# Kernel tuning notes

Measured on AMD Instinct MI355X. Metric: run time of the kernel, lower is better.

## Reference

```python
import jax, jax.numpy as jnp
import numpy as np

N_NODES = 50000
N_EDGES = 800000
IN_CH = 1024
OUT_CH = 256


def setup_inputs() -> dict:
    key = jax.random.key(0)
    ks = jax.random.split(key, 7)
    x = jax.random.normal(ks[0], (N_NODES, IN_CH), dtype=jnp.float32)
    src_index = jax.random.randint(ks[1], (N_EDGES,), 0, N_NODES, dtype=jnp.int32)
    tar_index = jax.random.randint(ks[2], (N_EDGES,), 0, N_NODES, dtype=jnp.int32)
    edge_weight = jax.random.uniform(ks[3], (N_EDGES,), dtype=jnp.float32)
    self_edge_weight = jax.random.uniform(ks[4], (N_NODES,), dtype=jnp.float32)
    # Linear layer params (torch.nn.Linear: y = x @ W.T + b)
    bound = 1.0 / np.sqrt(IN_CH)
    W = jax.random.uniform(ks[5], (OUT_CH, IN_CH), dtype=jnp.float32, minval=-bound, maxval=bound)
    b = jax.random.uniform(ks[6], (OUT_CH,), dtype=jnp.float32, minval=-bound, maxval=bound)
    return {"x": x, "W": W, "b": b, "src_index": src_index, "tar_index": tar_index,
            "edge_weight": edge_weight, "self_edge_weight": self_edge_weight}


def reference(x, W, b, src_index, tar_index, edge_weight, self_edge_weight):
    # dense linear projection: [N, in] -> [N, out]
    h = jnp.einsum('ni,oi->no', x, W) + b
    # edge aggregation: out[t] += w_e * h[src_e]  (SpMM-like gather/scatter)
    msgs = h[src_index] * edge_weight[:, None]          # [E, out]
    agg = jax.ops.segment_sum(msgs, tar_index, num_segments=h.shape[0])
    # self-loop term
    return agg + self_edge_weight[:, None] * h
```

## Files before the change

### kernel.cpp

```cpp
#include <hip/hip_runtime.h>
#include <hip/hip_bf16.h>

#define N_NODES 50000
#define N_EDGES 800000
#define IN_CH 1024
#define OUT_CH 256
#define NBLK 196

typedef __attribute__((ext_vector_type(8))) short bf16x8;
typedef __attribute__((ext_vector_type(4))) float f32x4;

__device__ inline unsigned short f2bf(float f) {
  union { float f; unsigned int u; } v; v.f = f;
  unsigned int r = v.u + 0x7fffu + ((v.u >> 16) & 1u);
  return (unsigned short)(r >> 16);
}
__device__ inline float bf2f(unsigned short u) {
  union { unsigned int u; float f; } v; v.u = ((unsigned int)u) << 16;
  return v.f;
}
__device__ inline unsigned int cvtpk_bf16(float a, float b) {
  unsigned int r;
  asm("v_cvt_pk_bf16_f32 %0, %1, %2" : "=v"(r) : "v"(a), "v"(b));
  return r;
}

#define GLOAD16(SRC, DST)                                                      \
  __builtin_amdgcn_global_load_lds(                                            \
      (const __attribute__((address_space(1))) void*)(SRC),                    \
      (__attribute__((address_space(3))) void*)(DST), 16, 0, 0)

__global__ __launch_bounds__(256) void prep_hist(const float* __restrict__ W,
                                                 unsigned short* __restrict__ Wb,
                                                 const int* __restrict__ tar,
                                                 int* __restrict__ counts) {
  const int b = blockIdx.x, t = threadIdx.x;
  if (b < 256) {
    const int i4 = (b * 256 + t) * 4;
    float4 f = *(const float4*)(W + i4);
    *(ushort4*)(Wb + i4) = make_ushort4(f2bf(f.x), f2bf(f.y), f2bf(f.z), f2bf(f.w));
  } else {
    const int e = (b - 256) * 256 + t;
    if (e < N_EDGES) atomicAdd(&counts[tar[e]], 1);
  }
}

__global__ __launch_bounds__(256, 3) void gemm_proj(
    const float* __restrict__ X, const unsigned short* __restrict__ Wb,
    const float* __restrict__ bias, unsigned short* __restrict__ Hb)
{
  __shared__ float lds_a[2][128][32];
  __shared__ unsigned short lds_b[2][128][32];

  const int tid  = threadIdx.x;
  const int lane = tid & 63;
  const int w    = tid >> 6;
  const int wr   = w >> 1, wc = w & 1;
  const int gm0  = blockIdx.x * 128;
  const int gn0  = blockIdx.y * 128;

  f32x4 acc[4][4];
  #pragma unroll
  for (int i = 0; i < 4; i++)
    #pragma unroll
    for (int j = 0; j < 4; j++) acc[i][j] = (f32x4)0.0f;

#define STAGE(BUF, K0)                                                         \
  {                                                                            \
    _Pragma("unroll")                                                          \
    for (int q = 0; q < 4; q++) {                                              \
      const int wl   = w * 4 + q;                                              \
      const int row  = 8 * wl + (lane >> 3);                                   \
      const int grow = gm0 + row;                                              \
      const int sc   = (lane & 7) ^ (row & 7);                                 \
      if (grow < N_NODES)                                                      \
        GLOAD16(X + (size_t)grow * IN_CH + (K0) + sc * 4,                      \
                &lds_a[BUF][8 * wl][0]);                                       \
    }                                                                          \
    _Pragma("unroll")                                                          \
    for (int q = 0; q < 2; q++) {                                              \
      const int wl  = w * 2 + q;                                               \
      const int row = 16 * wl + (lane >> 2);                                   \
      const int sc  = (lane & 3) ^ (row & 3);                                  \
      GLOAD16(Wb + (size_t)(gn0 + row) * IN_CH + (K0) + sc * 8,                \
              &lds_b[BUF][16 * wl][0]);                                        \
    }                                                                          \
  }

#define COMPUTE(BUF)                                                           \
  {                                                                            \
    const int l15 = lane & 15;                                                 \
    const int kb  = lane >> 4;                                                 \
    bf16x8 af[4], bfr[4];                                                      \
    _Pragma("unroll")                                                          \
    for (int i = 0; i < 4; i++) {                                              \
      const int row = wr * 64 + i * 16 + l15;                                  \
      const int c0  = (2 * kb) ^ (row & 7);                                    \
      const int c1  = (2 * kb + 1) ^ (row & 7);                                \
      f32x4 lo = *(const f32x4*)&lds_a[BUF][row][c0 * 4];                      \
      f32x4 hi = *(const f32x4*)&lds_a[BUF][row][c1 * 4];                      \
      union { unsigned int u[4]; bf16x8 v; } t;                                \
      t.u[0] = cvtpk_bf16(lo[0], lo[1]);                                       \
      t.u[1] = cvtpk_bf16(lo[2], lo[3]);                                       \
      t.u[2] = cvtpk_bf16(hi[0], hi[1]);                                       \
      t.u[3] = cvtpk_bf16(hi[2], hi[3]);                                       \
      af[i] = t.v;                                                             \
    }                                                                          \
    _Pragma("unroll")                                                          \
    for (int j = 0; j < 4; j++) {                                              \
      const int row = wc * 64 + j * 16 + l15;                                  \
      const int c   = kb ^ (row & 3);                                          \
      bfr[j] = *(const bf16x8*)&lds_b[BUF][row][c * 8];                        \
    }                                                                          \
    _Pragma("unroll")                                                          \
    for (int i = 0; i < 4; i++)                                                \
      _Pragma("unroll")                                                        \
      for (int j = 0; j < 4; j++)                                              \
        acc[i][j] = __builtin_amdgcn_mfma_f32_16x16x32_bf16(af[i], bfr[j],     \
                                                            acc[i][j], 0, 0, 0); \
  }

  STAGE(0, 0);
  __syncthreads();

  for (int ks = 0; ks < 32; ks += 2) {
    if (ks + 1 < 32) STAGE(1, (ks + 1) * 32);
    COMPUTE(0);
    __syncthreads();
    if (ks + 2 < 32) STAGE(0, (ks + 2) * 32);
    COMPUTE(1);
    __syncthreads();
  }
#undef STAGE
#undef COMPUTE

  float bj[4];
  #pragma unroll
  for (int j = 0; j < 4; j++)
    bj[j] = bias[gn0 + wc * 64 + j * 16 + (lane & 15)];

  #pragma unroll
  for (int i = 0; i < 4; i++) {
    const int grow_base = gm0 + wr * 64 + i * 16 + ((lane >> 4) << 2);
    #pragma unroll
    for (int r = 0; r < 4; r++) {
      const int grow = grow_base + r;
      if (grow < N_NODES) {
        #pragma unroll
        for (int j = 0; j < 4; j++) {
          const int gcol = gn0 + wc * 64 + j * 16 + (lane & 15);
          Hb[(size_t)grow * OUT_CH + gcol] = f2bf(acc[i][j][r] + bj[j]);
        }
      }
    }
  }
}

__global__ __launch_bounds__(256) void scan_block(const int* __restrict__ counts,
                                                  int* __restrict__ offsets,
                                                  int* __restrict__ blocksum) {
  __shared__ int wsum[4];
  const int tid = threadIdx.x, lane = tid & 63, wv = tid >> 6;
  const int i = blockIdx.x * 256 + tid;
  const int v = (i < N_NODES) ? counts[i] : 0;
  int s = v;
  #pragma unroll
  for (int off = 1; off < 64; off <<= 1) {
    int t = __shfl_up(s, off, 64);
    if (lane >= off) s += t;
  }
  if (lane == 63) wsum[wv] = s;
  __syncthreads();
  if (tid == 0) {
    int c = 0;
    #pragma unroll
    for (int k = 0; k < 4; k++) { int t = wsum[k]; wsum[k] = c; c += t; }
  }
  __syncthreads();
  const int excl = wsum[wv] + s - v;
  if (i < N_NODES) offsets[i] = excl;
  if (tid == 255) blocksum[blockIdx.x] = excl + v;
}

__global__ __launch_bounds__(256) void scan_sums(int* __restrict__ blocksum,
                                                 int* __restrict__ offsets) {
  __shared__ int wsum[4];
  const int tid = threadIdx.x, lane = tid & 63, wv = tid >> 6;
  const int v = (tid < NBLK) ? blocksum[tid] : 0;
  int s = v;
  #pragma unroll
  for (int off = 1; off < 64; off <<= 1) {
    int t = __shfl_up(s, off, 64);
    if (lane >= off) s += t;
  }
  if (lane == 63) wsum[wv] = s;
  __syncthreads();
  if (tid == 0) {
    int c = 0;
    #pragma unroll
    for (int k = 0; k < 4; k++) { int t = wsum[k]; wsum[k] = c; c += t; }
  }
  __syncthreads();
  const int excl = wsum[wv] + s - v;
  if (tid < NBLK) blocksum[tid] = excl;
  if (tid == 255) offsets[N_NODES] = excl;
}

__global__ __launch_bounds__(256) void finalize_offsets(int* __restrict__ offsets,
                                                        const int* __restrict__ blocksum,
                                                        int* __restrict__ cursor) {
  const int i = blockIdx.x * 256 + threadIdx.x;
  if (i < N_NODES) {
    const int off = offsets[i] + blocksum[i >> 8];
    offsets[i] = off;
    cursor[i] = off;
  }
}

__global__ __launch_bounds__(256) void fill_csr(const int* __restrict__ src,
                                                const int* __restrict__ tar,
                                                const float* __restrict__ ew,
                                                int* __restrict__ cursor,
                                                int2* __restrict__ edata) {
  int e = blockIdx.x * blockDim.x + threadIdx.x;
  if (e >= N_EDGES) return;
  const int t = tar[e];
  const int p = atomicAdd(&cursor[t], 1);
  edata[p] = make_int2(src[e], __float_as_int(ew[e]));
}

__global__ __launch_bounds__(256) void node_agg(
    const unsigned short* __restrict__ Hb, const int* __restrict__ offsets,
    const int2* __restrict__ edata, const float* __restrict__ sw,
    float* __restrict__ OUT)
{
  const int wid = (blockIdx.x * blockDim.x + threadIdx.x) >> 6;
  if (wid >= N_NODES) return;
  const int lane = threadIdx.x & 63;
  const int e0 = offsets[wid];
  const int e1 = offsets[wid + 1];

  float a0 = 0.f, a1 = 0.f, a2 = 0.f, a3 = 0.f;

  for (int base = e0; base < e1; base += 64) {
    const int avail = e1 - base;
    int2 d = make_int2(0, 0);
    if (lane < avail) d = edata[base + lane];
    const int n = (avail < 64) ? avail : 64;
    int j = 0;
    for (; j + 4 <= n; j += 4) {
      const int   s0 = __shfl(d.x, j, 64),     s1 = __shfl(d.x, j + 1, 64);
      const int   s2 = __shfl(d.x, j + 2, 64), s3 = __shfl(d.x, j + 3, 64);
      const float w0 = __int_as_float(__shfl(d.y, j, 64));
      const float w1 = __int_as_float(__shfl(d.y, j + 1, 64));
      const float w2 = __int_as_float(__shfl(d.y, j + 2, 64));
      const float w3 = __int_as_float(__shfl(d.y, j + 3, 64));
      const ushort4 h0 = *(const ushort4*)(Hb + (size_t)s0 * OUT_CH + lane * 4);
      const ushort4 h1 = *(const ushort4*)(Hb + (size_t)s1 * OUT_CH + lane * 4);
      const ushort4 h2 = *(const ushort4*)(Hb + (size_t)s2 * OUT_CH + lane * 4);
      const ushort4 h3 = *(const ushort4*)(Hb + (size_t)s3 * OUT_CH + lane * 4);
      a0 += w0 * bf2f(h0.x) + w1 * bf2f(h1.x) + w2 * bf2f(h2.x) + w3 * bf2f(h3.x);
      a1 += w0 * bf2f(h0.y) + w1 * bf2f(h1.y) + w2 * bf2f(h2.y) + w3 * bf2f(h3.y);
      a2 += w0 * bf2f(h0.z) + w1 * bf2f(h1.z) + w2 * bf2f(h2.z) + w3 * bf2f(h3.z);
      a3 += w0 * bf2f(h0.w) + w1 * bf2f(h1.w) + w2 * bf2f(h2.w) + w3 * bf2f(h3.w);
    }
    for (; j < n; j++) {
      const int   s = __shfl(d.x, j, 64);
      const float wgt = __int_as_float(__shfl(d.y, j, 64));
      const ushort4 h = *(const ushort4*)(Hb + (size_t)s * OUT_CH + lane * 4);
      a0 += wgt * bf2f(h.x); a1 += wgt * bf2f(h.y);
      a2 += wgt * bf2f(h.z); a3 += wgt * bf2f(h.w);
    }
  }

  const float swv = sw[wid];
  const ushort4 hs = *(const ushort4*)(Hb + (size_t)wid * OUT_CH + lane * 4);
  float4 o;
  o.x = a0 + swv * bf2f(hs.x);
  o.y = a1 + swv * bf2f(hs.y);
  o.z = a2 + swv * bf2f(hs.z);
  o.w = a3 + swv * bf2f(hs.w);
  *(float4*)(OUT + (size_t)wid * OUT_CH + lane * 4) = o;
}

extern "C" void kernel_launch(void* const* d_in, const int* in_sizes, int n_in,
                              void* d_out, int out_size, void* d_ws, size_t ws_size,
                              hipStream_t stream) {
  const float* x   = (const float*)d_in[0];
  const float* W   = (const float*)d_in[1];
  const float* b   = (const float*)d_in[2];
  const int*   src = (const int*)d_in[3];
  const int*   tar = (const int*)d_in[4];
  const float* ew  = (const float*)d_in[5];
  const float* sw  = (const float*)d_in[6];
  float* out = (float*)d_out;

  char* ws = (char*)d_ws;
  size_t o = 0;
  unsigned short* Wb = (unsigned short*)(ws + o);
  o += (size_t)OUT_CH * IN_CH * 2;          o = (o + 255) & ~(size_t)255;
  unsigned short* Hb = (unsigned short*)(ws + o);
  o += (size_t)N_NODES * OUT_CH * 2;        o = (o + 255) & ~(size_t)255;
  int* counts   = (int*)(ws + o); o += (size_t)N_NODES * 4;       o = (o + 255) & ~(size_t)255;
  int* offsets  = (int*)(ws + o); o += (size_t)(N_NODES + 1) * 4; o = (o + 255) & ~(size_t)255;
  int* cursor   = (int*)(ws + o); o += (size_t)N_NODES * 4;       o = (o + 255) & ~(size_t)255;
  int* blocksum = (int*)(ws + o); o += (size_t)NBLK * 4;          o = (o + 255) & ~(size_t)255;
  int2* edata   = (int2*)(ws + o);

  hipMemsetAsync(counts, 0, (size_t)N_NODES * 4, stream);
  prep_hist<<<256 + (N_EDGES + 255) / 256, 256, 0, stream>>>(W, Wb, tar, counts);
  scan_block<<<NBLK, 256, 0, stream>>>(counts, offsets, blocksum);
  scan_sums<<<1, 256, 0, stream>>>(blocksum, offsets);
  finalize_offsets<<<NBLK, 256, 0, stream>>>(offsets, blocksum, cursor);
  fill_csr<<<(N_EDGES + 255) / 256, 256, 0, stream>>>(src, tar, ew, cursor, edata);

  dim3 g1((N_NODES + 127) / 128, OUT_CH / 128);
  gemm_proj<<<g1, 256, 0, stream>>>(x, Wb, b, Hb);

  const long long nthreads = (long long)N_NODES * 64;
  node_agg<<<(int)((nthreads + 255) / 256), 256, 0, stream>>>(Hb, offsets, edata, sw, out);
}
```

Baseline: 248.4 us.

## Triple-buffer GEMM with vmcnt-based barriers and deepen SpMM gather unroll

The projection GEMM moves from double to triple LDS buffering and replaces full __syncthreads with partial s_waitcnt vmcnt(6) barriers, so two K-tiles of loads stay in flight while one is computed. Out-of-range rows are clamped instead of predicated, which keeps the count of outstanding loads uniform for the vmcnt accounting. Launch bounds drop to 2 blocks per SM because of the extra LDS. The aggregation kernel now issues 8 independent row gathers per iteration instead of 4, for more memory-level parallelism at some register cost.

```diff
diff --git a/kernel.cpp b/kernel.cpp
--- a/kernel.cpp
+++ b/kernel.cpp
@@ -29,6 +29,19 @@
   __builtin_amdgcn_global_load_lds(                                            \
       (const __attribute__((address_space(1))) void*)(SRC),                    \
       (__attribute__((address_space(3))) void*)(DST), 16, 0, 0)
+
+__device__ inline void waitbar6() {
+  __builtin_amdgcn_sched_barrier(0);
+  asm volatile("s_waitcnt vmcnt(6)" ::: "memory");
+  __builtin_amdgcn_s_barrier();
+  __builtin_amdgcn_sched_barrier(0);
+}
+__device__ inline void waitbar0() {
+  __builtin_amdgcn_sched_barrier(0);
+  asm volatile("s_waitcnt vmcnt(0)" ::: "memory");
+  __builtin_amdgcn_s_barrier();
+  __builtin_amdgcn_sched_barrier(0);
+}
 
 __global__ __launch_bounds__(256) void prep_hist(const float* __restrict__ W,
                                                  unsigned short* __restrict__ Wb,
@@ -45,12 +58,12 @@
   }
 }
 
-__global__ __launch_bounds__(256, 3) void gemm_proj(
+__global__ __launch_bounds__(256, 2) void gemm_proj(
     const float* __restrict__ X, const unsigned short* __restrict__ Wb,
     const float* __restrict__ bias, unsigned short* __restrict__ Hb)
 {
-  __shared__ float lds_a[2][128][32];
-  __shared__ unsigned short lds_b[2][128][32];
+  __shared__ float lds_a[3][128][32];
+  __shared__ unsigned short lds_b[3][128][32];
 
   const int tid  = threadIdx.x;
   const int lane = tid & 63;
@@ -69,13 +82,13 @@
   {                                                                            \
     _Pragma("unroll")                                                          \
     for (int q = 0; q < 4; q++) {                                              \
-      const int wl   = w * 4 + q;                                              \
-      const int row  = 8 * wl + (lane >> 3);                                   \
-      const int grow = gm0 + row;                                              \
-      const int sc   = (lane & 7) ^ (row & 7);                                 \
-      if (grow < N_NODES)                                                      \
-        GLOAD16(X + (size_t)grow * IN_CH + (K0) + sc * 4,                      \
-                &lds_a[BUF][8 * wl][0]);                                       \
+      const int wl  = w * 4 + q;                                               \
+      const int row = 8 * wl + (lane >> 3);                                    \
+      int grow = gm0 + row;                                                    \
+      if (grow > N_NODES - 1) grow = N_NODES - 1;                              \
+      const int sc = (lane & 7) ^ (row & 7);                                   \
+      GLOAD16(X + (size_t)grow * IN_CH + (K0) + sc * 4,                        \
+              &lds_a[BUF][8 * wl][0]);                                         \
     }                                                                          \
     _Pragma("unroll")                                                          \
     for (int q = 0; q < 2; q++) {                                              \
@@ -121,15 +134,15 @@
   }
 
   STAGE(0, 0);
-  __syncthreads();
-
-  for (int ks = 0; ks < 32; ks += 2) {
-    if (ks + 1 < 32) STAGE(1, (ks + 1) * 32);
-    COMPUTE(0);
-    __syncthreads();
-    if (ks + 2 < 32) STAGE(0, (ks + 2) * 32);
-    COMPUTE(1);
-    __syncthreads();
+  STAGE(1, 32);
+  waitbar6();
+
+  #pragma unroll
+  for (int t = 0; t < 32; t++) {
+    if (t + 2 < 32) STAGE((t + 2) % 3, (t + 2) * 32);
+    COMPUTE(t % 3);
+    if (t + 2 < 32)      waitbar6();
+    else if (t == 30)    waitbar0();
   }
 #undef STAGE
 #undef COMPUTE
@@ -248,21 +261,25 @@
     if (lane < avail) d = edata[base + lane];
     const int n = (avail < 64) ? avail : 64;
     int j = 0;
-    for (; j + 4 <= n; j += 4) {
-      const int   s0 = __shfl(d.x, j, 64),     s1 = __shfl(d.x, j + 1, 64);
-      const int   s2 = __shfl(d.x, j + 2, 64), s3 = __shfl(d.x, j + 3, 64);
-      const float w0 = __int_as_float(__shfl(d.y, j, 64));
-      const float w1 = __int_as_float(__shfl(d.y, j + 1, 64));
-      const float w2 = __int_as_float(__shfl(d.y, j + 2, 64));
-      const float w3 = __int_as_float(__shfl(d.y, j + 3, 64));
-      const ushort4 h0 = *(const ushort4*)(Hb + (size_t)s0 * OUT_CH + lane * 4);
-      const ushort4 h1 = *(const ushort4*)(Hb + (size_t)s1 * OUT_CH + lane * 4);
-      const ushort4 h2 = *(const ushort4*)(Hb + (size_t)s2 * OUT_CH + lane * 4);
-      const ushort4 h3 = *(const ushort4*)(Hb + (size_t)s3 * OUT_CH + lane * 4);
-      a0 += w0 * bf2f(h0.x) + w1 * bf2f(h1.x) + w2 * bf2f(h2.x) + w3 * bf2f(h3.x);
-      a1 += w0 * bf2f(h0.y) + w1 * bf2f(h1.y) + w2 * bf2f(h2.y) + w3 * bf2f(h3.y);
-      a2 += w0 * bf2f(h0.z) + w1 * bf2f(h1.z) + w2 * bf2f(h2.z) + w3 * bf2f(h3.z);
-      a3 += w0 * bf2f(h0.w) + w1 * bf2f(h1.w) + w2 * bf2f(h2.w) + w3 * bf2f(h3.w);
+    for (; j + 8 <= n; j += 8) {
+      int   sE[8];
+      float wE[8];
+      #pragma unroll
+      for (int q = 0; q < 8; q++) {
+        sE[q] = __shfl(d.x, j + q, 64);
+        wE[q] = __int_as_float(__shfl(d.y, j + q, 64));
+      }
+      ushort4 hE[8];
+      #pragma unroll
+      for (int q = 0; q < 8; q++)
+        hE[q] = *(const ushort4*)(Hb + (size_t)sE[q] * OUT_CH + lane * 4);
+      #pragma unroll
+      for (int q = 0; q < 8; q++) {
+        a0 += wE[q] * bf2f(hE[q].x);
+        a1 += wE[q] * bf2f(hE[q].y);
+        a2 += wE[q] * bf2f(hE[q].z);
+        a3 += wE[q] * bf2f(hE[q].w);
+      }
     }
     for (; j < n; j++) {
       const int   s = __shfl(d.x, j, 64);
```

Result: faster. 236.3 us (-4.9%).
